# Performance work log

Hardware: AMD Instinct MI355X
Metric: run time of the kernel (lower is better)

Reference implementation:

```python
import jax, jax.numpy as jnp
import numpy as np

B = 16384       # num graphs
N = 524288      # num atoms/nodes
E = 1048576     # num edges
D_EMB = 128     # dim_emb (atom embedding dim from mol_encoder)
D_STATE = 64    # dim_state
D_EDGE = 32     # raw edge_attr feature dim
N_STATES = 10   # dim_state_encoding (embedding vocab)


def setup_inputs() -> dict:
    key = jax.random.key(0)
    ks = jax.random.split(key, 11)
    return {
        "edge_attr": jax.random.normal(ks[0], (E, D_EDGE), dtype=jnp.float32),
        "z_mol": jax.random.normal(ks[1], (B, D_EMB), dtype=jnp.float32),
        "z_atom": jax.random.normal(ks[2], (N, D_EMB), dtype=jnp.float32),
        "state_emb": jax.random.normal(ks[3], (N_STATES, D_STATE), dtype=jnp.float32),
        "W1": jax.random.normal(ks[4], (D_EMB + D_STATE, 32), dtype=jnp.float32) * 0.07,
        "b1": jnp.zeros((32,), dtype=jnp.float32),
        "W2": jax.random.normal(ks[5], (32, 1), dtype=jnp.float32) * 0.18,
        "b2": jnp.zeros((1,), dtype=jnp.float32),
        "state": jax.random.randint(ks[6], (B,), 0, N_STATES),
        "edge_index0": jax.random.randint(ks[7], (E,), 0, N),
        "batch": jnp.sort(jax.random.randint(ks[8], (N,), 0, B)),
    }


def reference(edge_attr, z_mol, z_atom, state_emb, W1, b1, W2, b2,
              state, edge_index0, batch):
    # z_state = self.state_encoder(state)                     [B, Ds]
    z_state = state_emb[state]
    # gather per-node state embedding                         [N, Ds]
    z_state_nodes = z_state[batch]
    # edge_attr = cat([edge_attr, z_state[batch[edge_index[0]]]], 1)  [E, De+Ds]
    edge_attr_out = jnp.concatenate([edge_attr, z_state_nodes[edge_index0]], axis=1)
    # attn = fc_attn(cat([z_atom, z_state[batch]], 1))         [N, 1]
    h = jnp.concatenate([z_atom, z_state_nodes], axis=1)
    logits = jax.nn.leaky_relu(h @ W1 + b1, negative_slope=0.01) @ W2 + b2
    # segment softmax over graphs (PyG torch_geometric.utils.softmax)
    seg_max = jax.ops.segment_max(logits, batch, num_segments=B)   # [B, 1]
    ex = jnp.exp(logits - seg_max[batch])
    seg_sum = jax.ops.segment_sum(ex, batch, num_segments=B)       # [B, 1]
    attn = ex / (seg_sum[batch] + 1e-16)
    # z_mol_state = global_add_pool(attn * z_atom, batch)      [B, D_emb]
    z_mol_state = jax.ops.segment_sum(attn * z_atom, batch, num_segments=B)
    # input to spect_decoder (opaque downstream)               [B, 2*D_emb]
    x = jnp.concatenate([z_mol, z_mol_state], axis=1)
    return (x, edge_attr_out)
```

## Files before the change

### kernel.cpp

```cpp
#include <hip/hip_runtime.h>
#include <math.h>

#define B_GRAPHS 16384
#define N_NODES  524288
#define E_EDGES  1048576
#define D_EMB    128
#define D_STATE  64
#define HID      32
#define PADK     136
#define WPB      4
#define NWIN     (N_NODES / 32)
#define WIN_BLOCKS (NWIN / WPB)
#define NB_COPY    (E_EDGES * 8 / 256)
#define NB_STATE   (E_EDGES * 16 / 256)

typedef __attribute__((ext_vector_type(8))) short short8;
typedef __attribute__((ext_vector_type(4))) float f32x4;

__device__ __forceinline__ unsigned short f2bf(float f) {
    unsigned int u = __builtin_bit_cast(unsigned int, f);
    u += 0x7fffu + ((u >> 16) & 1u);
    return (unsigned short)(u >> 16);
}
__device__ __forceinline__ float bf2f(unsigned short s) {
    unsigned int u = ((unsigned int)s) << 16;
    return __builtin_bit_cast(float, u);
}

__global__ __launch_bounds__(256) void prep_kernel(
    const float* __restrict__ state_emb, const float* __restrict__ W1,
    const float* __restrict__ b1, const int* __restrict__ state,
    float* __restrict__ hb, f32x4* __restrict__ out_x4, f32x4* __restrict__ Sbuf4)
{
    const int bid = blockIdx.x, t = threadIdx.x;
    if (bid < 2048) {
        int j = t & 31;
        int g = bid * 8 + (t >> 5);
        int st = state[g];
        const float* zs = state_emb + st * D_STATE;
        float acc = b1[j];
        #pragma unroll 8
        for (int k = 0; k < D_STATE; ++k)
            acc += zs[k] * W1[(D_EMB + k) * HID + j];
        hb[g * HID + j] = acc;
    } else {
        int i = (bid - 2048) * 256 + t;
        int g = i >> 5, q = i & 31;
        f32x4 z = {0.f, 0.f, 0.f, 0.f};
        out_x4[(size_t)g * 64 + 32 + q] = z;
        if (i < B_GRAPHS / 4) Sbuf4[i] = z;
    }
}

__global__ __launch_bounds__(256, 4) void main_kernel(
    const float* __restrict__ z_atom,
    const float* __restrict__ W1,
    const float* __restrict__ W2,
    const float* __restrict__ b2,
    const int*   __restrict__ batch,
    const float* __restrict__ hb,
    float*       __restrict__ out_x,
    float*       __restrict__ Sbuf,
    const f32x4* __restrict__ edge_attr4,
    const f32x4* __restrict__ state_emb4,
    const int*   __restrict__ state,
    const int*   __restrict__ eidx,
    f32x4*       __restrict__ out_e4)
{
    __shared__ unsigned short s_zb[WPB][32][PADK];

    const int bid = blockIdx.x;
    const int t   = threadIdx.x;

    if (bid >= WIN_BLOCKS) {
        if (bid < WIN_BLOCKS + NB_COPY) {
            int tid = (bid - WIN_BLOCKS) * 256 + t;
            int e = tid >> 3, q = tid & 7;
            f32x4 v = __builtin_nontemporal_load(&edge_attr4[tid]);
            __builtin_nontemporal_store(v, &out_e4[(size_t)e * 24 + q]);
        } else {
            int tid = (bid - WIN_BLOCKS - NB_COPY) * 256 + t;
            int e = tid >> 4, q = tid & 15;
            int n = eidx[e];
            int b = batch[n];
            int s = state[b];
            f32x4 v = state_emb4[s * 16 + q];
            __builtin_nontemporal_store(v, &out_e4[(size_t)e * 24 + 8 + q]);
        }
        return;
    }

    const int lane = t & 63;
    const int w    = t >> 6;
    const int l15  = lane & 15;
    const int kc   = lane >> 4;

    short8 wa[2][4];
    #pragma unroll
    for (int jh = 0; jh < 2; ++jh)
        #pragma unroll
        for (int kb = 0; kb < 4; ++kb)
            #pragma unroll
            for (int i = 0; i < 8; ++i) {
                int k = kb * 32 + kc * 8 + i;
                wa[jh][kb][i] = (short)f2bf(W1[k * HID + jh * 16 + l15]);
            }

    const float b2v = b2[0];
    float w2v[2][4];
    #pragma unroll
    for (int jh = 0; jh < 2; ++jh)
        #pragma unroll
        for (int r = 0; r < 4; ++r)
            w2v[jh][r] = W2[16 * jh + 4 * kc + r];

    unsigned short (*zb)[PADK] = s_zb[w];

    const int win = bid * WPB + w;
    const int c0  = win * 32;
    int bv = 0;
    if (lane < 32) bv = batch[c0 + lane];

    const int leftN  = (c0 > 0) ? batch[c0 - 1] : -2;
    const int rightN = (c0 + 32 < N_NODES) ? batch[c0 + 32] : -2;

    float4 hbf[2][2];
    #pragma unroll
    for (int nh = 0; nh < 2; ++nh) {
        int bn = __shfl(bv, l15 + 16 * nh);
        hbf[nh][0] = *(const float4*)&hb[(size_t)bn * HID + 4 * kc];
        hbf[nh][1] = *(const float4*)&hb[(size_t)bn * HID + 16 + 4 * kc];
    }

    const f32x4* za4 = (const f32x4*)z_atom + (size_t)c0 * (D_EMB / 4);
    #pragma unroll
    for (int half = 0; half < 2; ++half) {
        f32x4 tmp[8];
        #pragma unroll
        for (int it = 0; it < 8; ++it) {
            int idx = (half * 8 + it) * 64 + lane;
            int n = idx >> 5, c = idx & 31;
            tmp[it] = __builtin_nontemporal_load(&za4[n * (D_EMB / 4) + c]);
        }
        #pragma unroll
        for (int it = 0; it < 8; ++it) {
            int idx = (half * 8 + it) * 64 + lane;
            int n = idx >> 5, c = idx & 31;
            f32x4 v = tmp[it];
            unsigned lo = (unsigned)f2bf(v[0]) | ((unsigned)f2bf(v[1]) << 16);
            unsigned hi = (unsigned)f2bf(v[2]) | ((unsigned)f2bf(v[3]) << 16);
            *(uint2*)&zb[n][c * 4] = make_uint2(lo, hi);
        }
    }

    f32x4 acc[2][2] = {{{0.f,0.f,0.f,0.f},{0.f,0.f,0.f,0.f}},
                       {{0.f,0.f,0.f,0.f},{0.f,0.f,0.f,0.f}}};
    #pragma unroll
    for (int kb = 0; kb < 4; ++kb) {
        short8 q0 = *(const short8*)&zb[l15][kb * 32 + kc * 8];
        short8 q1 = *(const short8*)&zb[16 + l15][kb * 32 + kc * 8];
        acc[0][0] = __builtin_amdgcn_mfma_f32_16x16x32_bf16(wa[0][kb], q0, acc[0][0], 0, 0, 0);
        acc[1][0] = __builtin_amdgcn_mfma_f32_16x16x32_bf16(wa[1][kb], q0, acc[1][0], 0, 0, 0);
        acc[0][1] = __builtin_amdgcn_mfma_f32_16x16x32_bf16(wa[0][kb], q1, acc[0][1], 0, 0, 0);
        acc[1][1] = __builtin_amdgcn_mfma_f32_16x16x32_bf16(wa[1][kb], q1, acc[1][1], 0, 0, 0);
    }

    float pt[2];
    #pragma unroll
    for (int nh = 0; nh < 2; ++nh) {
        float part = 0.f;
        #pragma unroll
        for (int r = 0; r < 4; ++r) {
            float h = acc[0][nh][r] + (&hbf[nh][0].x)[r];
            h = h > 0.f ? h : 0.01f * h;
            part += h * w2v[0][r];
        }
        #pragma unroll
        for (int r = 0; r < 4; ++r) {
            float h = acc[1][nh][r] + (&hbf[nh][1].x)[r];
            h = h > 0.f ? h : 0.01f * h;
            part += h * w2v[1][r];
        }
        part += __shfl_xor(part, 16);
        part += __shfl_xor(part, 32);
        pt[nh] = __expf(part + b2v);
    }

    float u0 = 0.f, u1 = 0.f, ss = 0.f;
    int cur = __shfl(bv, 0);
    int a = 0;

    #pragma unroll 4
    for (int n = 0; n < 32; ++n) {
        int bn = __shfl(bv, n);
        if (bn != cur) {
            if (a == 0 && leftN == cur) {
                atomicAdd(&out_x[(size_t)cur * 256 + 128 + lane * 2], u0);
                atomicAdd(&out_x[(size_t)cur * 256 + 129 + lane * 2], u1);
                if (lane == 0) atomicAdd(&Sbuf[cur], ss);
            } else {
                *(float2*)&out_x[(size_t)cur * 256 + 128 + lane * 2] = make_float2(u0, u1);
                if (lane == 0) Sbuf[cur] = ss;
            }
            u0 = u1 = ss = 0.f;
            cur = bn; a = n;
        }
        float pn = (n < 16) ? __shfl(pt[0], n) : __shfl(pt[1], n - 16);
        unsigned zz = *(const unsigned*)&zb[n][lane * 2];
        u0 += pn * bf2f((unsigned short)(zz & 0xffffu));
        u1 += pn * bf2f((unsigned short)(zz >> 16));
        ss += pn;
    }
    {
        bool lb = (a == 0) && (leftN == cur);
        bool rb = (rightN == cur);
        if (lb || rb) {
            atomicAdd(&out_x[(size_t)cur * 256 + 128 + lane * 2], u0);
            atomicAdd(&out_x[(size_t)cur * 256 + 129 + lane * 2], u1);
            if (lane == 0) atomicAdd(&Sbuf[cur], ss);
        } else {
            *(float2*)&out_x[(size_t)cur * 256 + 128 + lane * 2] = make_float2(u0, u1);
            if (lane == 0) Sbuf[cur] = ss;
        }
    }
}

__global__ __launch_bounds__(256) void finalize_kernel(
    const float* __restrict__ z_mol, const float* __restrict__ Sbuf,
    float* __restrict__ out_x)
{
    int i = blockIdx.x * 256 + threadIdx.x;
    int g = i >> 5, q = i & 31;
    f32x4 zm = *(const f32x4*)&z_mol[(size_t)g * D_EMB + q * 4];
    *(f32x4*)&out_x[(size_t)g * 256 + q * 4] = zm;
    float inv = 1.f / (Sbuf[g] + 1e-16f);
    f32x4 u = *(f32x4*)&out_x[(size_t)g * 256 + 128 + q * 4];
    u *= inv;
    *(f32x4*)&out_x[(size_t)g * 256 + 128 + q * 4] = u;
}

extern "C" void kernel_launch(void* const* d_in, const int* in_sizes, int n_in,
                              void* d_out, int out_size, void* d_ws, size_t ws_size,
                              hipStream_t stream)
{
    const float* edge_attr = (const float*)d_in[0];
    const float* z_mol     = (const float*)d_in[1];
    const float* z_atom    = (const float*)d_in[2];
    const float* state_emb = (const float*)d_in[3];
    const float* W1        = (const float*)d_in[4];
    const float* b1        = (const float*)d_in[5];
    const float* W2        = (const float*)d_in[6];
    const float* b2        = (const float*)d_in[7];
    const int*   state     = (const int*)d_in[8];
    const int*   eidx      = (const int*)d_in[9];
    const int*   batch     = (const int*)d_in[10];

    float* out_x = (float*)d_out;
    float* out_e = out_x + (size_t)B_GRAPHS * 256;

    float* hbuf = (float*)d_ws;
    float* Sbuf = (float*)((char*)d_ws + (size_t)B_GRAPHS * HID * 4);

    prep_kernel<<<4096, 256, 0, stream>>>(
        state_emb, W1, b1, state, hbuf, (f32x4*)out_x, (f32x4*)Sbuf);

    main_kernel<<<WIN_BLOCKS + NB_COPY + NB_STATE, 256, 0, stream>>>(
        z_atom, W1, W2, b2, batch, hbuf, out_x, Sbuf,
        (const f32x4*)edge_attr, (const f32x4*)state_emb, state, eidx,
        (f32x4*)out_e);

    finalize_kernel<<<(B_GRAPHS * 32) / 256, 256, 0, stream>>>(z_mol, Sbuf, out_x);
}
```

Before: 190.4 us.

## Move edge copy and state gather from window kernel into finalize kernel

```diff
diff --git a/kernel.cpp b/kernel.cpp
--- a/kernel.cpp
+++ b/kernel.cpp
@@ -11,6 +11,7 @@
 #define WPB      4
 #define NWIN     (N_NODES / 32)
 #define WIN_BLOCKS (NWIN / WPB)
+#define NB_FIN     (B_GRAPHS * 32 / 256)
 #define NB_COPY    (E_EDGES * 8 / 256)
 #define NB_STATE   (E_EDGES * 16 / 256)
 
@@ -52,7 +53,7 @@
     }
 }
 
-__global__ __launch_bounds__(256, 4) void main_kernel(
+__global__ __launch_bounds__(256, 4) void window_kernel(
     const float* __restrict__ z_atom,
     const float* __restrict__ W1,
     const float* __restrict__ W2,
@@ -60,36 +61,11 @@
     const int*   __restrict__ batch,
     const float* __restrict__ hb,
     float*       __restrict__ out_x,
-    float*       __restrict__ Sbuf,
-    const f32x4* __restrict__ edge_attr4,
-    const f32x4* __restrict__ state_emb4,
-    const int*   __restrict__ state,
-    const int*   __restrict__ eidx,
-    f32x4*       __restrict__ out_e4)
+    float*       __restrict__ Sbuf)
 {
     __shared__ unsigned short s_zb[WPB][32][PADK];
 
-    const int bid = blockIdx.x;
-    const int t   = threadIdx.x;
-
-    if (bid >= WIN_BLOCKS) {
-        if (bid < WIN_BLOCKS + NB_COPY) {
-            int tid = (bid - WIN_BLOCKS) * 256 + t;
-            int e = tid >> 3, q = tid & 7;
-            f32x4 v = __builtin_nontemporal_load(&edge_attr4[tid]);
-            __builtin_nontemporal_store(v, &out_e4[(size_t)e * 24 + q]);
-        } else {
-            int tid = (bid - WIN_BLOCKS - NB_COPY) * 256 + t;
-            int e = tid >> 4, q = tid & 15;
-            int n = eidx[e];
-            int b = batch[n];
-            int s = state[b];
-            f32x4 v = state_emb4[s * 16 + q];
-            __builtin_nontemporal_store(v, &out_e4[(size_t)e * 24 + 8 + q]);
-        }
-        return;
-    }
-
+    const int t    = threadIdx.x;
     const int lane = t & 63;
     const int w    = t >> 6;
     const int l15  = lane & 15;
@@ -116,7 +92,7 @@
 
     unsigned short (*zb)[PADK] = s_zb[w];
 
-    const int win = bid * WPB + w;
+    const int win = blockIdx.x * WPB + w;
     const int c0  = win * 32;
     int bv = 0;
     if (lane < 32) bv = batch[c0 + lane];
@@ -225,18 +201,41 @@
     }
 }
 
-__global__ __launch_bounds__(256) void finalize_kernel(
-    const float* __restrict__ z_mol, const float* __restrict__ Sbuf,
-    float* __restrict__ out_x)
-{
-    int i = blockIdx.x * 256 + threadIdx.x;
-    int g = i >> 5, q = i & 31;
-    f32x4 zm = *(const f32x4*)&z_mol[(size_t)g * D_EMB + q * 4];
-    *(f32x4*)&out_x[(size_t)g * 256 + q * 4] = zm;
-    float inv = 1.f / (Sbuf[g] + 1e-16f);
-    f32x4 u = *(f32x4*)&out_x[(size_t)g * 256 + 128 + q * 4];
-    u *= inv;
-    *(f32x4*)&out_x[(size_t)g * 256 + 128 + q * 4] = u;
+__global__ __launch_bounds__(256) void tail_kernel(
+    const float* __restrict__ z_mol,
+    const float* __restrict__ Sbuf,
+    float*       __restrict__ out_x,
+    const f32x4* __restrict__ edge_attr4,
+    const f32x4* __restrict__ state_emb4,
+    const int*   __restrict__ state,
+    const int*   __restrict__ eidx,
+    const int*   __restrict__ batch,
+    f32x4*       __restrict__ out_e4)
+{
+    const int bid = blockIdx.x, t = threadIdx.x;
+    if (bid < NB_FIN) {
+        int i = bid * 256 + t;
+        int g = i >> 5, q = i & 31;
+        f32x4 zm = *(const f32x4*)&z_mol[(size_t)g * D_EMB + q * 4];
+        *(f32x4*)&out_x[(size_t)g * 256 + q * 4] = zm;
+        float inv = 1.f / (Sbuf[g] + 1e-16f);
+        f32x4 u = *(f32x4*)&out_x[(size_t)g * 256 + 128 + q * 4];
+        u *= inv;
+        *(f32x4*)&out_x[(size_t)g * 256 + 128 + q * 4] = u;
+    } else if (bid < NB_FIN + NB_COPY) {
+        int tid = (bid - NB_FIN) * 256 + t;
+        int e = tid >> 3, q = tid & 7;
+        f32x4 v = __builtin_nontemporal_load(&edge_attr4[tid]);
+        __builtin_nontemporal_store(v, &out_e4[(size_t)e * 24 + q]);
+    } else {
+        int tid = (bid - NB_FIN - NB_COPY) * 256 + t;
+        int e = tid >> 4, q = tid & 15;
+        int n = eidx[e];
+        int b = batch[n];
+        int s = state[b];
+        f32x4 v = state_emb4[s * 16 + q];
+        __builtin_nontemporal_store(v, &out_e4[(size_t)e * 24 + 8 + q]);
+    }
 }
 
 extern "C" void kernel_launch(void* const* d_in, const int* in_sizes, int n_in,
@@ -264,10 +263,11 @@
     prep_kernel<<<4096, 256, 0, stream>>>(
         state_emb, W1, b1, state, hbuf, (f32x4*)out_x, (f32x4*)Sbuf);
 
-    main_kernel<<<WIN_BLOCKS + NB_COPY + NB_STATE, 256, 0, stream>>>(
-        z_atom, W1, W2, b2, batch, hbuf, out_x, Sbuf,
-        (const f32x4*)edge_attr, (const f32x4*)state_emb, state, eidx,
-        (f32x4*)out_e);
-
-    finalize_kernel<<<(B_GRAPHS * 32) / 256, 256, 0, stream>>>(z_mol, Sbuf, out_x);
-}
+    window_kernel<<<WIN_BLOCKS, 256, 0, stream>>>(
+        z_atom, W1, W2, b2, batch, hbuf, out_x, Sbuf);
+
+    tail_kernel<<<NB_FIN + NB_COPY + NB_STATE, 256, 0, stream>>>(
+        z_mol, Sbuf, out_x,
+        (const f32x4*)edge_attr, (const f32x4*)state_emb,
+        state, eidx, batch, (f32x4*)out_e);
+}
```

New measurement: 167.9 us (median of 2 runs). 1.13x faster.
